# Performance work log

Measured on AMD Instinct MI355X. Metric: run time of the kernel, lower is better.

The kernel has to match this reference:

```python
import jax, jax.numpy as jnp
import numpy as np

SCALE_VALUE = 1  # init kwarg; divide scores by sqrt(scale_value)


def setup_inputs() -> dict:
    key = jax.random.key(0)
    k1, k2 = jax.random.split(key)
    B, S, D = 8, 4096, 128
    inputs = jax.random.normal(k1, (B, S, D), dtype=jnp.float32)
    kernel = jax.random.normal(k2, (3, D, D), dtype=jnp.float32) * 0.05
    return {"inputs": inputs, "kernel": kernel}


def reference(inputs, kernel):
    # Q/K/V projections: [B,S,D] @ [D,D]
    wq = jnp.einsum('bsd,de->bse', inputs, kernel[0])
    wk = jnp.einsum('bsd,de->bse', inputs, kernel[1])
    wv = jnp.einsum('bsd,de->bse', inputs, kernel[2])
    # full attention score matrix [B,S,S], scaled by 1/sqrt(scale_value)
    qk = jnp.einsum('bqd,bkd->bqk', wq, wk) / (SCALE_VALUE ** 0.5)
    attn = jax.nn.softmax(qk, axis=-1)
    v = jnp.einsum('bqk,bkd->bqd', attn, wv)
    # mean pool over sequence -> [B,D]
    return jnp.mean(v, axis=1)
```

## Files before the change

kernel.cpp:

```cpp
#include <hip/hip_runtime.h>
#include <hip/hip_bf16.h>

#define Bsz 8
#define Ssz 4096
#define Dsz 128

typedef short bf16x8 __attribute__((ext_vector_type(8)));
typedef short bf16x4 __attribute__((ext_vector_type(4)));
typedef float f32x4 __attribute__((ext_vector_type(4)));

__device__ __forceinline__ short f2bf(float f) {
  union { float f; unsigned u; } v; v.f = f;
  unsigned r = v.u + 0x7fffu + ((v.u >> 16) & 1u);
  return (short)(r >> 16);
}

__device__ __forceinline__ void gll16(const void* g, void* l) {
  __builtin_amdgcn_global_load_lds((const __attribute__((address_space(1))) void*)g,
                                   (__attribute__((address_space(3))) void*)l, 16, 0, 0);
}


__global__ __launch_bounds__(256) void proj_kernel(
    const float* __restrict__ x, const float* __restrict__ w,
    short* __restrict__ Qs, short* __restrict__ Ks, short* __restrict__ Vs) {
  __shared__ short xb[16384];
  __shared__ short wb[16384];

  const int mat = blockIdx.x;
  const int rb = blockIdx.y;
  const int t = threadIdx.x;
  const int lane = t & 63;
  const int wv = t >> 6;
  const int quad = lane >> 4;
  const int l15 = lane & 15;
  const int wq = wv & 1, wk = wv >> 1;
  const float wscale = (mat == 0) ? 1.44269504088896340736f : 1.0f;

  {
    const float* xsrc = x + (size_t)rb * 128 * Dsz;
    #pragma unroll
    for (int p = 0; p < 16; ++p) {
      int idx4 = p * 256 + t;
      int row = idx4 >> 5;
      int d0 = (idx4 & 31) << 2;
      f32x4 v = *(const f32x4*)&xsrc[idx4 * 4];
      bf16x4 o;
      o[0] = f2bf(v[0]); o[1] = f2bf(v[1]); o[2] = f2bf(v[2]); o[3] = f2bf(v[3]);
      *(bf16x4*)&xb[(d0 >> 3) * 1024 + row * 8 + (d0 & 7)] = o;
    }
  }
  {
    const float* wsrc = w + (size_t)mat * Dsz * Dsz;
    #pragma unroll
    for (int p = 0; p < 16; ++p) {
      int idx4 = p * 256 + t;
      int d = idx4 >> 5;
      int e0 = (idx4 & 31) << 2;
      f32x4 v = *(const f32x4*)&wsrc[idx4 * 4];
      int base = (d >> 3) * 1024 + (d & 7);
      wb[base + (e0 + 0) * 8] = f2bf(v[0] * wscale);
      wb[base + (e0 + 1) * 8] = f2bf(v[1] * wscale);
      wb[base + (e0 + 2) * 8] = f2bf(v[2] * wscale);
      wb[base + (e0 + 3) * 8] = f2bf(v[3] * wscale);
    }
  }
  __syncthreads();

  f32x4 acc[4][4];
  #pragma unroll
  for (int mi = 0; mi < 4; ++mi)
    #pragma unroll
    for (int ni = 0; ni < 4; ++ni) acc[mi][ni] = (f32x4){0.f, 0.f, 0.f, 0.f};

  #pragma unroll
  for (int kc = 0; kc < 4; ++kc) {
    int g = kc * 4 + quad;
    bf16x8 af[4], bf[4];
    #pragma unroll
    for (int mi = 0; mi < 4; ++mi)
      af[mi] = *(const bf16x8*)&xb[g * 1024 + (wq * 64 + mi * 16 + l15) * 8];
    #pragma unroll
    for (int ni = 0; ni < 4; ++ni)
      bf[ni] = *(const bf16x8*)&wb[g * 1024 + (wk * 64 + ni * 16 + l15) * 8];
    #pragma unroll
    for (int mi = 0; mi < 4; ++mi)
      #pragma unroll
      for (int ni = 0; ni < 4; ++ni)
        acc[mi][ni] = __builtin_amdgcn_mfma_f32_16x16x32_bf16(af[mi], bf[ni], acc[mi][ni], 0, 0, 0);
  }
  __syncthreads();

  if (mat < 2) {
    #pragma unroll
    for (int mi = 0; mi < 4; ++mi)
      #pragma unroll
      for (int ni = 0; ni < 4; ++ni) {
        int e = wk * 64 + ni * 16 + l15;
        int base = (e >> 3) * 1024 + (e & 7);
        #pragma unroll
        for (int r = 0; r < 4; ++r) {
          int s = wq * 64 + mi * 16 + quad * 4 + r;
          xb[base + s * 8] = f2bf(acc[mi][ni][r]);
        }
      }
  } else {
    #pragma unroll
    for (int mi = 0; mi < 4; ++mi)
      #pragma unroll
      for (int ni = 0; ni < 4; ++ni) {
        int d = wk * 64 + ni * 16 + l15;
        int sbase = wq * 64 + mi * 16;
        int gs = (sbase >> 3) + (quad >> 1);
        bf16x4 o;
        o[0] = f2bf(acc[mi][ni][0]); o[1] = f2bf(acc[mi][ni][1]);
        o[2] = f2bf(acc[mi][ni][2]); o[3] = f2bf(acc[mi][ni][3]);
        *(bf16x4*)&xb[gs * 1024 + d * 8 + (quad & 1) * 4] = o;
      }
  }
  __syncthreads();

  short* dst = (mat == 0 ? Qs : (mat == 1 ? Ks : Vs)) + (size_t)rb * 16384;
  #pragma unroll
  for (int p = 0; p < 8; ++p) {
    int c = p * 256 + t;
    *(bf16x8*)&dst[c * 8] = *(const bf16x8*)&xb[c * 8];
  }
}

__global__ __launch_bounds__(256, 2) void attn_kernel(
    const short* __restrict__ Qs, const short* __restrict__ Ks,
    const short* __restrict__ Vs, float* __restrict__ acc_out) {
  __shared__ short kbuf[16384];
  __shared__ short vbuf[16384];
  __shared__ short pbuf[8192];

  const int b = blockIdx.x;
  const int qt = blockIdx.y;
  const int t = threadIdx.x;
  const int wv = t >> 6;
  const int lane = t & 63;
  const int quad = lane >> 4;
  const int l15 = lane & 15;
  const int wk = wv;

  bf16x8 aq[4][4];
  {
    const short* qsrc = Qs + (size_t)(b * 32 + (qt >> 1)) * 16384;
    const int qbase = (qt & 1) * 64;
    #pragma unroll
    for (int mi = 0; mi < 4; ++mi)
      #pragma unroll
      for (int kc = 0; kc < 4; ++kc)
        aq[mi][kc] = *(const bf16x8*)&qsrc[((kc * 4 + quad) * 128 + qbase + mi * 16 + l15) * 8];
  }

  f32x4 of[4][2];
  float rs[4][4];
  #pragma unroll
  for (int mi = 0; mi < 4; ++mi) {
    #pragma unroll
    for (int ni = 0; ni < 2; ++ni) of[mi][ni] = (f32x4){0.f, 0.f, 0.f, 0.f};
    #pragma unroll
    for (int r = 0; r < 4; ++r) rs[mi][r] = 0.f;
  }

  const short* kt_src = Ks + (size_t)b * 32 * 16384;
  const short* vt_src = Vs + (size_t)b * 32 * 16384;

  for (int it = 0; it < 32; ++it) {
    {
      const char* ksrc = (const char*)(kt_src + (size_t)it * 16384);
      const char* vsrc = (const char*)(vt_src + (size_t)it * 16384);
      #pragma unroll
      for (int p = 0; p < 8; ++p) {
        int c = wk * 8 + p;
        gll16(ksrc + c * 1024 + lane * 16, (char*)kbuf + c * 1024);
        gll16(vsrc + c * 1024 + lane * 16, (char*)vbuf + c * 1024);
      }
    }
    __syncthreads();

    f32x4 sc[4][2];
    #pragma unroll
    for (int mi = 0; mi < 4; ++mi)
      #pragma unroll
      for (int ni = 0; ni < 2; ++ni) sc[mi][ni] = (f32x4){0.f, 0.f, 0.f, 0.f};

    #pragma unroll
    for (int kc = 0; kc < 4; ++kc) {
      bf16x8 kf[2];
      #pragma unroll
      for (int ni = 0; ni < 2; ++ni)
        kf[ni] = *(const bf16x8*)&kbuf[(kc * 4 + quad) * 1024 + (wk * 32 + ni * 16 + l15) * 8];
      #pragma unroll
      for (int mi = 0; mi < 4; ++mi)
        #pragma unroll
        for (int ni = 0; ni < 2; ++ni)
          sc[mi][ni] = __builtin_amdgcn_mfma_f32_16x16x32_bf16(aq[mi][kc], kf[ni], sc[mi][ni], 0, 0, 0);
    }

    #pragma unroll
    for (int mi = 0; mi < 4; ++mi)
      #pragma unroll
      for (int ni = 0; ni < 2; ++ni) {
        int k = wk * 32 + ni * 16 + l15;
        int base = (k >> 3) * 512 + (k & 7);
        #pragma unroll
        for (int r = 0; r < 4; ++r) {
          float p = __builtin_amdgcn_exp2f(sc[mi][ni][r]);
          rs[mi][r] += p;
          int q = mi * 16 + quad * 4 + r;
          pbuf[base + q * 8] = f2bf(p);
        }
      }
    __syncthreads();

    #pragma unroll
    for (int kc = 0; kc < 4; ++kc) {
      bf16x8 pa[4], vf[2];
      #pragma unroll
      for (int mi = 0; mi < 4; ++mi)
        pa[mi] = *(const bf16x8*)&pbuf[(kc * 4 + quad) * 512 + (mi * 16 + l15) * 8];
      #pragma unroll
      for (int ni = 0; ni < 2; ++ni)
        vf[ni] = *(const bf16x8*)&vbuf[(kc * 4 + quad) * 1024 + (wk * 32 + ni * 16 + l15) * 8];
      #pragma unroll
      for (int mi = 0; mi < 4; ++mi)
        #pragma unroll
        for (int ni = 0; ni < 2; ++ni)
          of[mi][ni] = __builtin_amdgcn_mfma_f32_16x16x32_bf16(pa[mi], vf[ni], of[mi][ni], 0, 0, 0);
    }
    __syncthreads();
  }

  #pragma unroll
  for (int mi = 0; mi < 4; ++mi)
    #pragma unroll
    for (int r = 0; r < 4; ++r) {
      float v = rs[mi][r];
      v += __shfl_xor(v, 1, 64);
      v += __shfl_xor(v, 2, 64);
      v += __shfl_xor(v, 4, 64);
      v += __shfl_xor(v, 8, 64);
      rs[mi][r] = v;
    }
  float* rsf = (float*)pbuf;
  if (l15 == 0) {
    #pragma unroll
    for (int mi = 0; mi < 4; ++mi)
      #pragma unroll
      for (int r = 0; r < 4; ++r)
        rsf[(mi * 16 + quad * 4 + r) * 4 + wk] = rs[mi][r];
  }
  __syncthreads();

  float inv[4][4];
  #pragma unroll
  for (int mi = 0; mi < 4; ++mi)
    #pragma unroll
    for (int r = 0; r < 4; ++r) {
      int q = mi * 16 + quad * 4 + r;
      float l = rsf[q * 4] + rsf[q * 4 + 1] + rsf[q * 4 + 2] + rsf[q * 4 + 3];
      inv[mi][r] = 1.f / (l * (float)Ssz);
    }

  #pragma unroll
  for (int ni = 0; ni < 2; ++ni) {
    float cs = 0.f;
    #pragma unroll
    for (int mi = 0; mi < 4; ++mi)
      #pragma unroll
      for (int r = 0; r < 4; ++r)
        cs += of[mi][ni][r] * inv[mi][r];
    cs += __shfl_xor(cs, 16, 64);
    cs += __shfl_xor(cs, 32, 64);
    if (lane < 16)
      atomicAdd(&acc_out[b * Dsz + wk * 32 + ni * 16 + lane], cs);
  }
}

__global__ void finalize_kernel(const float* __restrict__ acc, float* __restrict__ out) {
  int i = blockIdx.x * 256 + threadIdx.x;
  if (i < Bsz * Dsz) out[i] = acc[i];
}

extern "C" void kernel_launch(void* const* d_in, const int* in_sizes, int n_in,
                              void* d_out, int out_size, void* d_ws, size_t ws_size,
                              hipStream_t stream) {
  const float* x = (const float*)d_in[0];
  const float* w = (const float*)d_in[1];
  short* Qs = (short*)d_ws;
  short* Ks = Qs + (size_t)Bsz * Ssz * Dsz;
  short* Vs = Ks + (size_t)Bsz * Ssz * Dsz;
  float* acc = (float*)(Vs + (size_t)Bsz * Ssz * Dsz);

  proj_kernel<<<dim3(3, 256), dim3(256), 0, stream>>>(x, w, Qs, Ks, Vs);
  hipMemsetAsync(acc, 0, Bsz * Dsz * sizeof(float), stream);
  attn_kernel<<<dim3(Bsz, 64), dim3(256), 0, stream>>>(Qs, Ks, Vs, acc);
  finalize_kernel<<<dim3((Bsz * Dsz + 255) / 256), dim3(256), 0, stream>>>(acc, (float*)d_out);
}
```

Before: 174.3 us.

## Restructure projection and attention kernels with pre-packed weights and double-buffered KV

Adds a small kernel that converts the weights to bf16 in MFMA layout once. The projection now computes Q, K and V in one block per row tile, so x is converted only once. The attention kernel moves to 128-query tiles per block with 64-key steps, double-buffers K/V loads through global_load_lds so the next tile loads during compute, and uses a padded row-major P buffer. Rounding now uses a cheaper packed conversion with round-half-away instead of round-to-nearest-even. The trade-offs are lower occupancy (launch bounds 1) and more registers for holding Q.

```diff
diff --git a/kernel.cpp b/kernel.cpp
--- a/kernel.cpp
+++ b/kernel.cpp
@@ -1,18 +1,19 @@
 #include <hip/hip_runtime.h>
-#include <hip/hip_bf16.h>
 
 #define Bsz 8
 #define Ssz 4096
 #define Dsz 128
 
 typedef short bf16x8 __attribute__((ext_vector_type(8)));
-typedef short bf16x4 __attribute__((ext_vector_type(4)));
 typedef float f32x4 __attribute__((ext_vector_type(4)));
-
-__device__ __forceinline__ short f2bf(float f) {
-  union { float f; unsigned u; } v; v.f = f;
-  unsigned r = v.u + 0x7fffu + ((v.u >> 16) & 1u);
-  return (short)(r >> 16);
+typedef int int2v __attribute__((ext_vector_type(2)));
+typedef int int4v __attribute__((ext_vector_type(4)));
+typedef unsigned int u32;
+
+__device__ __forceinline__ int pkbf(float a, float b) {
+  u32 ra = __float_as_uint(a) + 0x8000u;
+  u32 rb = __float_as_uint(b) + 0x8000u;
+  return (int)__builtin_amdgcn_perm(rb, ra, 0x07060302u);
 }
 
 __device__ __forceinline__ void gll16(const void* g, void* l) {
@@ -21,262 +22,275 @@
 }
 
 
+__global__ void wt_kernel(const float* __restrict__ w, short* __restrict__ Wt) {
+  int g = blockIdx.x * 256 + threadIdx.x;
+  int mat = g >> 11;
+  int rem = g & 2047;
+  int gd = rem >> 7;
+  int e = rem & 127;
+  float sc = (mat == 0) ? 1.44269504088896340736f : 1.0f;
+  const float* src = w + mat * Dsz * Dsz + gd * 8 * Dsz + e;
+  int pk[4];
+  #pragma unroll
+  for (int j = 0; j < 4; ++j)
+    pk[j] = pkbf(src[(2 * j) * Dsz] * sc, src[(2 * j + 1) * Dsz] * sc);
+  *(int4v*)&Wt[(size_t)g * 8] = *(const int4v*)pk;
+}
+
 __global__ __launch_bounds__(256) void proj_kernel(
-    const float* __restrict__ x, const float* __restrict__ w,
+    const float* __restrict__ x, const short* __restrict__ Wt,
     short* __restrict__ Qs, short* __restrict__ Ks, short* __restrict__ Vs) {
-  __shared__ short xb[16384];
+  __shared__ short xb[128 * 136];
   __shared__ short wb[16384];
-
-  const int mat = blockIdx.x;
-  const int rb = blockIdx.y;
+  __shared__ short ob[16384];
+
+  const int rb = blockIdx.x;
   const int t = threadIdx.x;
-  const int lane = t & 63;
-  const int wv = t >> 6;
-  const int quad = lane >> 4;
-  const int l15 = lane & 15;
-  const int wq = wv & 1, wk = wv >> 1;
-  const float wscale = (mat == 0) ? 1.44269504088896340736f : 1.0f;
+  const int lane = t & 63, wv = t >> 6;
+  const int quad = lane >> 4, l15 = lane & 15;
+  const int h0 = wv & 1, h1 = wv >> 1;
 
   {
     const float* xsrc = x + (size_t)rb * 128 * Dsz;
     #pragma unroll
     for (int p = 0; p < 16; ++p) {
       int idx4 = p * 256 + t;
-      int row = idx4 >> 5;
-      int d0 = (idx4 & 31) << 2;
+      int row = idx4 >> 5, d0 = (idx4 & 31) << 2;
       f32x4 v = *(const f32x4*)&xsrc[idx4 * 4];
-      bf16x4 o;
-      o[0] = f2bf(v[0]); o[1] = f2bf(v[1]); o[2] = f2bf(v[2]); o[3] = f2bf(v[3]);
-      *(bf16x4*)&xb[(d0 >> 3) * 1024 + row * 8 + (d0 & 7)] = o;
-    }
-  }
-  {
-    const float* wsrc = w + (size_t)mat * Dsz * Dsz;
-    #pragma unroll
-    for (int p = 0; p < 16; ++p) {
-      int idx4 = p * 256 + t;
-      int d = idx4 >> 5;
-      int e0 = (idx4 & 31) << 2;
-      f32x4 v = *(const f32x4*)&wsrc[idx4 * 4];
-      int base = (d >> 3) * 1024 + (d & 7);
-      wb[base + (e0 + 0) * 8] = f2bf(v[0] * wscale);
-      wb[base + (e0 + 1) * 8] = f2bf(v[1] * wscale);
-      wb[base + (e0 + 2) * 8] = f2bf(v[2] * wscale);
-      wb[base + (e0 + 3) * 8] = f2bf(v[3] * wscale);
-    }
-  }
-  __syncthreads();
-
-  f32x4 acc[4][4];
-  #pragma unroll
-  for (int mi = 0; mi < 4; ++mi)
-    #pragma unroll
-    for (int ni = 0; ni < 4; ++ni) acc[mi][ni] = (f32x4){0.f, 0.f, 0.f, 0.f};
-
-  #pragma unroll
-  for (int kc = 0; kc < 4; ++kc) {
-    int g = kc * 4 + quad;
-    bf16x8 af[4], bf[4];
-    #pragma unroll
-    for (int mi = 0; mi < 4; ++mi)
-      af[mi] = *(const bf16x8*)&xb[g * 1024 + (wq * 64 + mi * 16 + l15) * 8];
-    #pragma unroll
-    for (int ni = 0; ni < 4; ++ni)
-      bf[ni] = *(const bf16x8*)&wb[g * 1024 + (wk * 64 + ni * 16 + l15) * 8];
-    #pragma unroll
-    for (int mi = 0; mi < 4; ++mi)
-      #pragma unroll
-      for (int ni = 0; ni < 4; ++ni)
-        acc[mi][ni] = __builtin_amdgcn_mfma_f32_16x16x32_bf16(af[mi], bf[ni], acc[mi][ni], 0, 0, 0);
-  }
-  __syncthreads();
-
-  if (mat < 2) {
-    #pragma unroll
-    for (int mi = 0; mi < 4; ++mi)
-      #pragma unroll
-      for (int ni = 0; ni < 4; ++ni) {
-        int e = wk * 64 + ni * 16 + l15;
-        int base = (e >> 3) * 1024 + (e & 7);
-        #pragma unroll
-        for (int r = 0; r < 4; ++r) {
-          int s = wq * 64 + mi * 16 + quad * 4 + r;
-          xb[base + s * 8] = f2bf(acc[mi][ni][r]);
+      int2v pr;
+      pr[0] = pkbf(v[0], v[1]);
+      pr[1] = pkbf(v[2], v[3]);
+      *(int2v*)&xb[row * 136 + d0] = pr;
+    }
+  }
+
+  for (int mat = 0; mat < 3; ++mat) {
+    {
+      const char* wsrc = (const char*)(Wt + (size_t)mat * 16384);
+      #pragma unroll
+      for (int i = 0; i < 8; ++i) {
+        int p = wv * 8 + i;
+        gll16(wsrc + p * 1024 + lane * 16, (char*)wb + p * 1024);
+      }
+    }
+    __syncthreads();
+
+    f32x4 acc[4][4];
+    #pragma unroll
+    for (int a = 0; a < 4; ++a)
+      #pragma unroll
+      for (int c = 0; c < 4; ++c) acc[a][c] = (f32x4){0.f, 0.f, 0.f, 0.f};
+
+    if (mat < 2) {
+      #pragma unroll
+      for (int kc = 0; kc < 4; ++kc) {
+        bf16x8 aw[4], bx[4];
+        #pragma unroll
+        for (int me = 0; me < 4; ++me)
+          aw[me] = *(const bf16x8*)&wb[(kc * 4 + quad) * 1024 + (h0 * 64 + me * 16 + l15) * 8];
+        #pragma unroll
+        for (int ns = 0; ns < 4; ++ns)
+          bx[ns] = *(const bf16x8*)&xb[(h1 * 64 + ns * 16 + l15) * 136 + kc * 32 + quad * 8];
+        #pragma unroll
+        for (int me = 0; me < 4; ++me)
+          #pragma unroll
+          for (int ns = 0; ns < 4; ++ns)
+            acc[me][ns] = __builtin_amdgcn_mfma_f32_16x16x32_bf16(aw[me], bx[ns], acc[me][ns], 0, 0, 0);
+      }
+      __syncthreads();
+      #pragma unroll
+      for (int me = 0; me < 4; ++me)
+        #pragma unroll
+        for (int ns = 0; ns < 4; ++ns) {
+          int e0 = h0 * 64 + me * 16 + quad * 4;
+          int s = h1 * 64 + ns * 16 + l15;
+          int2v pr;
+          pr[0] = pkbf(acc[me][ns][0], acc[me][ns][1]);
+          pr[1] = pkbf(acc[me][ns][2], acc[me][ns][3]);
+          *(int2v*)&ob[(e0 >> 3) * 1024 + s * 8 + (e0 & 7)] = pr;
         }
+    } else {
+      #pragma unroll
+      for (int kc = 0; kc < 4; ++kc) {
+        bf16x8 ax[4], bw[4];
+        #pragma unroll
+        for (int ms = 0; ms < 4; ++ms)
+          ax[ms] = *(const bf16x8*)&xb[(h0 * 64 + ms * 16 + l15) * 136 + kc * 32 + quad * 8];
+        #pragma unroll
+        for (int ne = 0; ne < 4; ++ne)
+          bw[ne] = *(const bf16x8*)&wb[(kc * 4 + quad) * 1024 + (h1 * 64 + ne * 16 + l15) * 8];
+        #pragma unroll
+        for (int ms = 0; ms < 4; ++ms)
+          #pragma unroll
+          for (int ne = 0; ne < 4; ++ne)
+            acc[ms][ne] = __builtin_amdgcn_mfma_f32_16x16x32_bf16(ax[ms], bw[ne], acc[ms][ne], 0, 0, 0);
       }
-  } else {
-    #pragma unroll
-    for (int mi = 0; mi < 4; ++mi)
-      #pragma unroll
-      for (int ni = 0; ni < 4; ++ni) {
-        int d = wk * 64 + ni * 16 + l15;
-        int sbase = wq * 64 + mi * 16;
-        int gs = (sbase >> 3) + (quad >> 1);
-        bf16x4 o;
-        o[0] = f2bf(acc[mi][ni][0]); o[1] = f2bf(acc[mi][ni][1]);
-        o[2] = f2bf(acc[mi][ni][2]); o[3] = f2bf(acc[mi][ni][3]);
-        *(bf16x4*)&xb[gs * 1024 + d * 8 + (quad & 1) * 4] = o;
-      }
-  }
-  __syncthreads();
-
-  short* dst = (mat == 0 ? Qs : (mat == 1 ? Ks : Vs)) + (size_t)rb * 16384;
-  #pragma unroll
-  for (int p = 0; p < 8; ++p) {
-    int c = p * 256 + t;
-    *(bf16x8*)&dst[c * 8] = *(const bf16x8*)&xb[c * 8];
-  }
-}
-
-__global__ __launch_bounds__(256, 2) void attn_kernel(
+      __syncthreads();
+      #pragma unroll
+      for (int ms = 0; ms < 4; ++ms)
+        #pragma unroll
+        for (int ne = 0; ne < 4; ++ne) {
+          int s0 = h0 * 64 + ms * 16 + quad * 4;
+          int e = h1 * 64 + ne * 16 + l15;
+          int2v pr;
+          pr[0] = pkbf(acc[ms][ne][0], acc[ms][ne][1]);
+          pr[1] = pkbf(acc[ms][ne][2], acc[ms][ne][3]);
+          *(int2v*)&ob[(s0 >> 3) * 1024 + e * 8 + (s0 & 7)] = pr;
+        }
+    }
+    __syncthreads();
+    short* dst = (mat == 0 ? Qs : (mat == 1 ? Ks : Vs)) + (size_t)rb * 16384;
+    #pragma unroll
+    for (int p = 0; p < 8; ++p) {
+      int c = p * 256 + t;
+      *(int4v*)&dst[c * 8] = *(const int4v*)&ob[c * 8];
+    }
+  }
+}
+
+__global__ __launch_bounds__(256, 1) void attn_kernel(
     const short* __restrict__ Qs, const short* __restrict__ Ks,
     const short* __restrict__ Vs, float* __restrict__ acc_out) {
-  __shared__ short kbuf[16384];
-  __shared__ short vbuf[16384];
-  __shared__ short pbuf[8192];
+  __shared__ short kbuf[2][8192];
+  __shared__ short vbuf[2][8192];
+  __shared__ short pbuf[128 * 72];
+  __shared__ float rsbuf[128 * 4];
+  __shared__ float linv[128];
 
   const int b = blockIdx.x;
   const int qt = blockIdx.y;
   const int t = threadIdx.x;
-  const int wv = t >> 6;
+  const int w = t >> 6;
   const int lane = t & 63;
-  const int quad = lane >> 4;
-  const int l15 = lane & 15;
-  const int wk = wv;
-
-  bf16x8 aq[4][4];
+  const int quad = lane >> 4, l15 = lane & 15;
+  const int qh = w >> 1, dh = w & 1;
+
+  bf16x8 aq[8][4];
   {
-    const short* qsrc = Qs + (size_t)(b * 32 + (qt >> 1)) * 16384;
-    const int qbase = (qt & 1) * 64;
-    #pragma unroll
-    for (int mi = 0; mi < 4; ++mi)
+    const short* qsrc = Qs + (size_t)(b * 32 + qt) * 16384;
+    #pragma unroll
+    for (int nq = 0; nq < 8; ++nq)
       #pragma unroll
       for (int kc = 0; kc < 4; ++kc)
-        aq[mi][kc] = *(const bf16x8*)&qsrc[((kc * 4 + quad) * 128 + qbase + mi * 16 + l15) * 8];
-  }
-
-  f32x4 of[4][2];
-  float rs[4][4];
-  #pragma unroll
-  for (int mi = 0; mi < 4; ++mi) {
-    #pragma unroll
-    for (int ni = 0; ni < 2; ++ni) of[mi][ni] = (f32x4){0.f, 0.f, 0.f, 0.f};
-    #pragma unroll
-    for (int r = 0; r < 4; ++r) rs[mi][r] = 0.f;
-  }
-
-  const short* kt_src = Ks + (size_t)b * 32 * 16384;
-  const short* vt_src = Vs + (size_t)b * 32 * 16384;
-
-  for (int it = 0; it < 32; ++it) {
-    {
-      const char* ksrc = (const char*)(kt_src + (size_t)it * 16384);
-      const char* vsrc = (const char*)(vt_src + (size_t)it * 16384);
-      #pragma unroll
-      for (int p = 0; p < 8; ++p) {
-        int c = wk * 8 + p;
-        gll16(ksrc + c * 1024 + lane * 16, (char*)kbuf + c * 1024);
-        gll16(vsrc + c * 1024 + lane * 16, (char*)vbuf + c * 1024);
-      }
+        aq[nq][kc] = *(const bf16x8*)&qsrc[((kc * 4 + quad) * 128 + nq * 16 + l15) * 8];
+  }
+
+  f32x4 of[4][4];
+  float rs[8];
+  #pragma unroll
+  for (int mq = 0; mq < 4; ++mq)
+    #pragma unroll
+    for (int nd = 0; nd < 4; ++nd) of[mq][nd] = (f32x4){0.f, 0.f, 0.f, 0.f};
+  #pragma unroll
+  for (int nq = 0; nq < 8; ++nq) rs[nq] = 0.f;
+
+  const char* kbase = (const char*)(Ks + (size_t)b * 32 * 16384);
+  const char* vbase = (const char*)(Vs + (size_t)b * 32 * 16384);
+
+  #define STAGE(it_, bf_)                                                              \
+    {                                                                                  \
+      int tile_ = (it_) >> 1, half_ = (it_) & 1;                                       \
+      const char* ks_ = kbase + (size_t)tile_ * 32768;                                 \
+      const char* vs_ = vbase + (size_t)tile_ * 32768 + half_ * 16384;                 \
+      _Pragma("unroll")                                                                \
+      for (int i_ = 0; i_ < 8; ++i_) {                                                 \
+        int p_ = w * 8 + i_;                                                           \
+        if (p_ < 16)                                                                   \
+          gll16(ks_ + p_ * 2048 + half_ * 1024 + lane * 16, (char*)kbuf[bf_] + p_ * 1024); \
+        else                                                                           \
+          gll16(vs_ + (p_ - 16) * 1024 + lane * 16, (char*)vbuf[bf_] + (p_ - 16) * 1024);  \
+      }                                                                                \
+    }
+
+  STAGE(0, 0);
+  __syncthreads();
+
+  for (int it = 0; it < 64; ++it) {
+    const int cur = it & 1;
+    if (it < 63) STAGE(it + 1, cur ^ 1);
+
+    f32x4 sc[8];
+    #pragma unroll
+    for (int nq = 0; nq < 8; ++nq) sc[nq] = (f32x4){0.f, 0.f, 0.f, 0.f};
+    #pragma unroll
+    for (int kc = 0; kc < 4; ++kc) {
+      bf16x8 akf = *(const bf16x8*)&kbuf[cur][(kc * 4 + quad) * 512 + (w * 16 + l15) * 8];
+      #pragma unroll
+      for (int nq = 0; nq < 8; ++nq)
+        sc[nq] = __builtin_amdgcn_mfma_f32_16x16x32_bf16(akf, aq[nq][kc], sc[nq], 0, 0, 0);
+    }
+
+    const int k0 = w * 16 + quad * 4;
+    #pragma unroll
+    for (int nq = 0; nq < 8; ++nq) {
+      float p0 = __builtin_amdgcn_exp2f(sc[nq][0]);
+      float p1 = __builtin_amdgcn_exp2f(sc[nq][1]);
+      float p2 = __builtin_amdgcn_exp2f(sc[nq][2]);
+      float p3 = __builtin_amdgcn_exp2f(sc[nq][3]);
+      rs[nq] += (p0 + p1) + (p2 + p3);
+      int2v pr;
+      pr[0] = pkbf(p0, p1);
+      pr[1] = pkbf(p2, p3);
+      *(int2v*)&pbuf[(nq * 16 + l15) * 72 + k0] = pr;
     }
     __syncthreads();
 
-    f32x4 sc[4][2];
-    #pragma unroll
-    for (int mi = 0; mi < 4; ++mi)
-      #pragma unroll
-      for (int ni = 0; ni < 2; ++ni) sc[mi][ni] = (f32x4){0.f, 0.f, 0.f, 0.f};
-
-    #pragma unroll
-    for (int kc = 0; kc < 4; ++kc) {
-      bf16x8 kf[2];
-      #pragma unroll
-      for (int ni = 0; ni < 2; ++ni)
-        kf[ni] = *(const bf16x8*)&kbuf[(kc * 4 + quad) * 1024 + (wk * 32 + ni * 16 + l15) * 8];
-      #pragma unroll
-      for (int mi = 0; mi < 4; ++mi)
-        #pragma unroll
-        for (int ni = 0; ni < 2; ++ni)
-          sc[mi][ni] = __builtin_amdgcn_mfma_f32_16x16x32_bf16(aq[mi][kc], kf[ni], sc[mi][ni], 0, 0, 0);
-    }
-
-    #pragma unroll
-    for (int mi = 0; mi < 4; ++mi)
-      #pragma unroll
-      for (int ni = 0; ni < 2; ++ni) {
-        int k = wk * 32 + ni * 16 + l15;
-        int base = (k >> 3) * 512 + (k & 7);
-        #pragma unroll
-        for (int r = 0; r < 4; ++r) {
-          float p = __builtin_amdgcn_exp2f(sc[mi][ni][r]);
-          rs[mi][r] += p;
-          int q = mi * 16 + quad * 4 + r;
-          pbuf[base + q * 8] = f2bf(p);
-        }
-      }
+    #pragma unroll
+    for (int kc2 = 0; kc2 < 2; ++kc2) {
+      bf16x8 pa[4], vf[4];
+      #pragma unroll
+      for (int mq = 0; mq < 4; ++mq)
+        pa[mq] = *(const bf16x8*)&pbuf[(qh * 64 + mq * 16 + l15) * 72 + kc2 * 32 + quad * 8];
+      #pragma unroll
+      for (int nd = 0; nd < 4; ++nd)
+        vf[nd] = *(const bf16x8*)&vbuf[cur][(kc2 * 4 + quad) * 1024 + (dh * 64 + nd * 16 + l15) * 8];
+      #pragma unroll
+      for (int mq = 0; mq < 4; ++mq)
+        #pragma unroll
+        for (int nd = 0; nd < 4; ++nd)
+          of[mq][nd] = __builtin_amdgcn_mfma_f32_16x16x32_bf16(pa[mq], vf[nd], of[mq][nd], 0, 0, 0);
+    }
     __syncthreads();
-
-    #pragma unroll
-    for (int kc = 0; kc < 4; ++kc) {
-      bf16x8 pa[4], vf[2];
-      #pragma unroll
-      for (int mi = 0; mi < 4; ++mi)
-        pa[mi] = *(const bf16x8*)&pbuf[(kc * 4 + quad) * 512 + (mi * 16 + l15) * 8];
-      #pragma unroll
-      for (int ni = 0; ni < 2; ++ni)
-        vf[ni] = *(const bf16x8*)&vbuf[(kc * 4 + quad) * 1024 + (wk * 32 + ni * 16 + l15) * 8];
-      #pragma unroll
-      for (int mi = 0; mi < 4; ++mi)
-        #pragma unroll
-        for (int ni = 0; ni < 2; ++ni)
-          of[mi][ni] = __builtin_amdgcn_mfma_f32_16x16x32_bf16(pa[mi], vf[ni], of[mi][ni], 0, 0, 0);
-    }
-    __syncthreads();
-  }
-
-  #pragma unroll
-  for (int mi = 0; mi < 4; ++mi)
-    #pragma unroll
-    for (int r = 0; r < 4; ++r) {
-      float v = rs[mi][r];
-      v += __shfl_xor(v, 1, 64);
-      v += __shfl_xor(v, 2, 64);
-      v += __shfl_xor(v, 4, 64);
-      v += __shfl_xor(v, 8, 64);
-      rs[mi][r] = v;
-    }
-  float* rsf = (float*)pbuf;
-  if (l15 == 0) {
-    #pragma unroll
-    for (int mi = 0; mi < 4; ++mi)
+  }
+
+  #pragma unroll
+  for (int nq = 0; nq < 8; ++nq) {
+    float v = rs[nq];
+    v += __shfl_xor(v, 16, 64);
+    v += __shfl_xor(v, 32, 64);
+    rs[nq] = v;
+  }
+  if (lane < 16) {
+    #pragma unroll
+    for (int nq = 0; nq < 8; ++nq)
+      rsbuf[(nq * 16 + l15) * 4 + w] = rs[nq];
+  }
+  __syncthreads();
+  if (t < 128) {
+    float l = rsbuf[t * 4] + rsbuf[t * 4 + 1] + rsbuf[t * 4 + 2] + rsbuf[t * 4 + 3];
+    linv[t] = 1.f / (l * (float)Ssz);
+  }
+  __syncthreads();
+
+  float li[4][4];
+  #pragma unroll
+  for (int mq = 0; mq < 4; ++mq)
+    #pragma unroll
+    for (int r = 0; r < 4; ++r)
+      li[mq][r] = linv[qh * 64 + mq * 16 + quad * 4 + r];
+
+  #pragma unroll
+  for (int nd = 0; nd < 4; ++nd) {
+    float cs = 0.f;
+    #pragma unroll
+    for (int mq = 0; mq < 4; ++mq)
       #pragma unroll
       for (int r = 0; r < 4; ++r)
-        rsf[(mi * 16 + quad * 4 + r) * 4 + wk] = rs[mi][r];
-  }
-  __syncthreads();
-
-  float inv[4][4];
-  #pragma unroll
-  for (int mi = 0; mi < 4; ++mi)
-    #pragma unroll
-    for (int r = 0; r < 4; ++r) {
-      int q = mi * 16 + quad * 4 + r;
-      float l = rsf[q * 4] + rsf[q * 4 + 1] + rsf[q * 4 + 2] + rsf[q * 4 + 3];
-      inv[mi][r] = 1.f / (l * (float)Ssz);
-    }
-
-  #pragma unroll
-  for (int ni = 0; ni < 2; ++ni) {
-    float cs = 0.f;
-    #pragma unroll
-    for (int mi = 0; mi < 4; ++mi)
-      #pragma unroll
-      for (int r = 0; r < 4; ++r)
-        cs += of[mi][ni][r] * inv[mi][r];
+        cs += of[mq][nd][r] * li[mq][r];
     cs += __shfl_xor(cs, 16, 64);
     cs += __shfl_xor(cs, 32, 64);
     if (lane < 16)
-      atomicAdd(&acc_out[b * Dsz + wk * 32 + ni * 16 + lane], cs);
+      atomicAdd(&acc_out[b * Dsz + dh * 64 + nd * 16 + l15], cs);
   }
 }
 
@@ -294,9 +308,11 @@
   short* Ks = Qs + (size_t)Bsz * Ssz * Dsz;
   short* Vs = Ks + (size_t)Bsz * Ssz * Dsz;
   float* acc = (float*)(Vs + (size_t)Bsz * Ssz * Dsz);
-
-  proj_kernel<<<dim3(3, 256), dim3(256), 0, stream>>>(x, w, Qs, Ks, Vs);
+  short* Wt = (short*)(acc + Bsz * Dsz);
+
+  wt_kernel<<<dim3(24), dim3(256), 0, stream>>>(w, Wt);
   hipMemsetAsync(acc, 0, Bsz * Dsz * sizeof(float), stream);
-  attn_kernel<<<dim3(Bsz, 64), dim3(256), 0, stream>>>(Qs, Ks, Vs, acc);
+  proj_kernel<<<dim3(256), dim3(256), 0, stream>>>(x, Wt, Qs, Ks, Vs);
+  attn_kernel<<<dim3(Bsz, Ssz / 128), dim3(256), 0, stream>>>(Qs, Ks, Vs, acc);
   finalize_kernel<<<dim3((Bsz * Dsz + 255) / 256), dim3(256), 0, stream>>>(acc, (float*)d_out);
 }
```

After: 188.4 us. 8.1% more time.
